# Kernel optimization log

Measured on AMD Instinct MI355X. Metric: run time of the kernel, lower is better.

The kernel has to match this reference:

```python
import jax, jax.numpy as jnp
import numpy as np

# Haar (db1) decomposition filters, pywt convention
_S = 1.0 / np.sqrt(2.0)
# dec_lo = [s, s], dec_hi = [-s, s]. Each scalar input v becomes signal [v, 0]
# (zero-pad to 2**dwt_level = 2). The single valid DWT coeff (mode='zero') is
#   cA = v * dec_lo[1] = v * s ;  cD = v * dec_hi[1] = v * s
CA_COEF = np.float32(_S)   # dec_lo[1]
CD_COEF = np.float32(_S)   # dec_hi[1]

B, N, F, OUT = 8, 20000, 256, 256
WAVELET_FULL_LEN = 2  # len(cA) + len(cD) for level-1 db1 on length-2 signal


def setup_inputs() -> dict:
    key = jax.random.key(0)
    kx, kw, kb, kwo, kbo = jax.random.split(key, 5)
    x = jax.random.normal(kx, (B, N, F), dtype=jnp.float32)
    # per-feature nn.Linear(wavelet_full_len, 1) stacked: weight [F, 2], bias [F]
    lim_nl = 1.0 / np.sqrt(WAVELET_FULL_LEN)
    W_nl = jax.random.uniform(kw, (F, WAVELET_FULL_LEN), jnp.float32, -lim_nl, lim_nl)
    b_nl = jax.random.uniform(kb, (F,), jnp.float32, -lim_nl, lim_nl)
    # linear_out: [out_dim, feat_dim] torch layout, bias [out_dim]
    lim_o = 1.0 / np.sqrt(F)
    W_out = jax.random.uniform(kwo, (OUT, F), jnp.float32, -lim_o, lim_o)
    b_out = jax.random.uniform(kbo, (OUT,), jnp.float32, -lim_o, lim_o)
    return {"x": x, "W_nl": W_nl, "b_nl": b_nl, "W_out": W_out, "b_out": b_out}


def reference(x, W_nl, b_nl, W_out, b_out):
    # Batched wavelet features: for each scalar, coeffs are [cA, cD] = [s*v, s*v]
    # feat_wave: [B, N, F, 2]
    feat_wave = jnp.stack([x * CA_COEF, x * CD_COEF], axis=-1)
    # Per-feature Linear(2, 1), batched over the feature dim
    agg_nl = jnp.einsum("bnfk,fk->bnf", feat_wave, W_nl) + b_nl  # [B, N, F]
    # Output linear (dropout is identity in eval)
    out = jnp.einsum("bnf,of->bno", agg_nl, W_out) + b_out  # [B, N, OUT]
    return out
```

## Files before the change

kernel.cpp:

```cpp
#include <hip/hip_runtime.h>

typedef __bf16 bf16x8 __attribute__((ext_vector_type(8)));
typedef __bf16 bf16x4 __attribute__((ext_vector_type(4)));
typedef float f32x4 __attribute__((ext_vector_type(4)));

__device__ __forceinline__ unsigned short f2b(float f) {
    unsigned int u = __float_as_uint(f);
    return (unsigned short)((u + 0x7fffu + ((u >> 16) & 1u)) >> 16);
}

__global__ __launch_bounds__(256) void wk_prep(
    const float* __restrict__ Wnl, const float* __restrict__ bnl,
    const float* __restrict__ Wout, const float* __restrict__ bout,
    unsigned short* __restrict__ wfrag, float* __restrict__ wbias) {
    int b = blockIdx.x, tid = threadIdx.x;
    if (b < 256) {
        int t = b * 256 + tid;
        int j = t & 7;
        int lane = (t >> 3) & 63;
        int ks = (t >> 9) & 7;
        int ct = t >> 12;
        int f = ks * 32 + ((lane >> 4) << 3) + j;
        int o = ct * 16 + (lane & 15);
        float c = 0.70710678f * (Wnl[2 * f] + Wnl[2 * f + 1]);
        wfrag[t] = f2b(c * Wout[o * 256 + f]);
    } else {
        int o = tid;
        const float4* wr = (const float4*)(Wout + o * 256);
        const float4* bn = (const float4*)bnl;
        float s = 0.f;
        #pragma unroll 4
        for (int i = 0; i < 64; ++i) {
            float4 a = bn[i], b4 = wr[i];
            s += a.x * b4.x + a.y * b4.y + a.z * b4.z + a.w * b4.w;
        }
        wbias[o] = bout[o] + s;
    }
}

__global__ __launch_bounds__(512, 4) void wk_main(
    const float* __restrict__ x, const unsigned short* __restrict__ wfrag,
    const float* __restrict__ wbias, float* __restrict__ out) {
    const int tid  = threadIdx.x;
    const int lane = tid & 63;
    const int w    = tid >> 6;
    const int m    = lane & 15;
    const int quad = lane >> 4;

    __shared__ char Xlds[2][18432];

    const int b  = blockIdx.x;
    const int t0 = (b * 5000) >> 9;
    const int t1 = ((b + 1) * 5000) >> 9;

    int4  Wf[2][8];
    f32x4 bias[2];
    {
        const int4* ws = (const int4*)wfrag;
        #pragma unroll
        for (int c2 = 0; c2 < 2; ++c2) {
            #pragma unroll
            for (int ks = 0; ks < 8; ++ks)
                Wf[c2][ks] = ws[(((2 * w + c2) * 8 + ks) << 6) + lane];
            bias[c2] = *(const f32x4*)(wbias + (2 * w + c2) * 16 + quad * 4);
        }
    }

    f32x4 sbuf[4];
    #define LOADT(T)                                                          \
        {                                                                     \
            const f32x4* xt = (const f32x4*)x + (size_t)(T) * 2048;           \
            _Pragma("unroll")                                                 \
            for (int s = 0; s < 4; ++s)                                       \
                sbuf[s] = xt[s * 512 + w * 64 + lane];                        \
        }

    LOADT(t0);
    int p = 0;
    for (int t = t0; t < t1; ++t) {
        {
            char* dst = Xlds[p] + w * 576 + lane * 8;
            #pragma unroll
            for (int s = 0; s < 4; ++s) {
                f32x4 u = sbuf[s];
                bf16x4 h;
                h[0] = (__bf16)u[0]; h[1] = (__bf16)u[1];
                h[2] = (__bf16)u[2]; h[3] = (__bf16)u[3];
                *(bf16x4*)(dst + s * 4608) = h;
            }
        }
        if (t + 1 < t1) LOADT(t + 1);
        asm volatile("s_waitcnt lgkmcnt(0)" ::: "memory");
        __builtin_amdgcn_s_barrier();
        __builtin_amdgcn_sched_barrier(0);

        const char* src = Xlds[p] + m * 576 + quad * 16;
        #pragma unroll
        for (int mt = 0; mt < 2; ++mt) {
            f32x4 a0 = bias[0], a1 = bias[1];
            #pragma unroll
            for (int ks = 0; ks < 8; ++ks) {
                bf16x8 afr = *(const bf16x8*)(src + mt * 9216 + ks * 64);
                a0 = __builtin_amdgcn_mfma_f32_16x16x32_bf16(
                    __builtin_bit_cast(bf16x8, Wf[0][ks]), afr, a0, 0, 0, 0);
                a1 = __builtin_amdgcn_mfma_f32_16x16x32_bf16(
                    __builtin_bit_cast(bf16x8, Wf[1][ks]), afr, a1, 0, 0, 0);
            }
            float* op = out + (size_t)(t * 32 + mt * 16 + m) * 256 + w * 32 + quad * 4;
            *(f32x4*)op        = a0;
            *(f32x4*)(op + 16) = a1;
        }
        p ^= 1;
    }
    #undef LOADT
}

extern "C" void kernel_launch(void* const* d_in, const int* in_sizes, int n_in,
                              void* d_out, int out_size, void* d_ws, size_t ws_size,
                              hipStream_t stream) {
    const float* x    = (const float*)d_in[0];
    const float* Wnl  = (const float*)d_in[1];
    const float* bnl  = (const float*)d_in[2];
    const float* Wout = (const float*)d_in[3];
    const float* bout = (const float*)d_in[4];

    unsigned short* wfrag = (unsigned short*)d_ws;
    float* wbias = (float*)((char*)d_ws + 131072);

    wk_prep<<<257, 256, 0, stream>>>(Wnl, bnl, Wout, bout, wfrag, wbias);
    wk_main<<<512, 512, 0, stream>>>(x, wfrag, wbias, (float*)d_out);
}
```

Measured before the change: 302.4 us.

## Prefetch two tiles ahead and stage outputs through LDS for coalesced stores

Doubles the register prefetch depth so global loads of x are issued two tiles ahead, using two alternating register buffers and a manually unrolled loop. MFMA results are written to a swizzled LDS buffer and then read back, so each wave stores full contiguous rows of the output instead of scattered 16-byte fragments. This aims to hide load latency and coalesce the dominant output writes, at the cost of an extra barrier per tile, 32KB more LDS per block (which may lower occupancy), and more registers. The prefetch of t0+1 is unconditional, which could read past the block's range when it has only one tile.

```diff
diff --git a/kernel.cpp b/kernel.cpp
--- a/kernel.cpp
+++ b/kernel.cpp
@@ -48,6 +48,7 @@
     const int quad = lane >> 4;
 
     __shared__ char Xlds[2][18432];
+    __shared__ char Olds[32768];
 
     const int b  = blockIdx.x;
     const int t0 = (b * 5000) >> 9;
@@ -66,52 +67,87 @@
         }
     }
 
-    f32x4 sbuf[4];
-    #define LOADT(T)                                                          \
+    f32x4 sbufA[4], sbufB[4];
+    #define LOADT(SB, T)                                                      \
         {                                                                     \
             const f32x4* xt = (const f32x4*)x + (size_t)(T) * 2048;           \
             _Pragma("unroll")                                                 \
             for (int s = 0; s < 4; ++s)                                       \
-                sbuf[s] = xt[s * 512 + w * 64 + lane];                        \
+                SB[s] = xt[s * 512 + w * 64 + lane];                          \
         }
 
-    LOADT(t0);
+    LOADT(sbufA, t0);
+    LOADT(sbufB, t0 + 1);
+
     int p = 0;
-    for (int t = t0; t < t1; ++t) {
-        {
-            char* dst = Xlds[p] + w * 576 + lane * 8;
-            #pragma unroll
-            for (int s = 0; s < 4; ++s) {
-                f32x4 u = sbuf[s];
-                bf16x4 h;
-                h[0] = (__bf16)u[0]; h[1] = (__bf16)u[1];
-                h[2] = (__bf16)u[2]; h[3] = (__bf16)u[3];
-                *(bf16x4*)(dst + s * 4608) = h;
-            }
-        }
-        if (t + 1 < t1) LOADT(t + 1);
-        asm volatile("s_waitcnt lgkmcnt(0)" ::: "memory");
-        __builtin_amdgcn_s_barrier();
-        __builtin_amdgcn_sched_barrier(0);
+    int t = t0;
 
-        const char* src = Xlds[p] + m * 576 + quad * 16;
-        #pragma unroll
-        for (int mt = 0; mt < 2; ++mt) {
-            f32x4 a0 = bias[0], a1 = bias[1];
-            #pragma unroll
-            for (int ks = 0; ks < 8; ++ks) {
-                bf16x8 afr = *(const bf16x8*)(src + mt * 9216 + ks * 64);
-                a0 = __builtin_amdgcn_mfma_f32_16x16x32_bf16(
-                    __builtin_bit_cast(bf16x8, Wf[0][ks]), afr, a0, 0, 0, 0);
-                a1 = __builtin_amdgcn_mfma_f32_16x16x32_bf16(
-                    __builtin_bit_cast(bf16x8, Wf[1][ks]), afr, a1, 0, 0, 0);
-            }
-            float* op = out + (size_t)(t * 32 + mt * 16 + m) * 256 + w * 32 + quad * 4;
-            *(f32x4*)op        = a0;
-            *(f32x4*)(op + 16) = a1;
-        }
-        p ^= 1;
+    #define STEP(SB)                                                          \
+    {                                                                         \
+              \
+        {                                                                     \
+            char* dst = Xlds[p] + w * 576 + lane * 8;                         \
+            _Pragma("unroll")                                                 \
+            for (int s = 0; s < 4; ++s) {                                     \
+                f32x4 u = SB[s];                                              \
+                bf16x4 h;                                                     \
+                h[0] = (__bf16)u[0]; h[1] = (__bf16)u[1];                     \
+                h[2] = (__bf16)u[2]; h[3] = (__bf16)u[3];                     \
+                *(bf16x4*)(dst + s * 4608) = h;                               \
+            }                                                                 \
+        }                                                                     \
+        if (t + 2 < t1) LOADT(SB, t + 2);               \
+        asm volatile("s_waitcnt lgkmcnt(0)" ::: "memory");                    \
+        __builtin_amdgcn_s_barrier();                                         \
+        __builtin_amdgcn_sched_barrier(0);                                    \
+                              \
+        {                                                                     \
+            const char* src = Xlds[p] + m * 576 + quad * 16;                  \
+            _Pragma("unroll")                                                 \
+            for (int mt = 0; mt < 2; ++mt) {                                  \
+                f32x4 a0 = bias[0], a1 = bias[1];                             \
+                _Pragma("unroll")                                             \
+                for (int ks = 0; ks < 8; ++ks) {                              \
+                    bf16x8 afr = *(const bf16x8*)(src + mt * 9216 + ks * 64); \
+                    a0 = __builtin_amdgcn_mfma_f32_16x16x32_bf16(             \
+                        __builtin_bit_cast(bf16x8, Wf[0][ks]), afr, a0,0,0,0);\
+                    a1 = __builtin_amdgcn_mfma_f32_16x16x32_bf16(             \
+                        __builtin_bit_cast(bf16x8, Wf[1][ks]), afr, a1,0,0,0);\
+                }                                                             \
+                const int S0 = 2 * w, S1 = 2 * w + 1;                         \
+                *(f32x4*)(Olds + ((S0 * 2048 + mt * 1024 + lane * 16)         \
+                                  ^ ((S0 & 7) << 4))) = a0;                   \
+                *(f32x4*)(Olds + ((S1 * 2048 + mt * 1024 + lane * 16)         \
+                                  ^ ((S1 & 7) << 4))) = a1;                   \
+            }                                                                 \
+        }                                                                     \
+        asm volatile("s_waitcnt lgkmcnt(0)" ::: "memory");                    \
+        __builtin_amdgcn_s_barrier();                                         \
+        __builtin_amdgcn_sched_barrier(0);                                    \
+          \
+        {                                                                     \
+            float* ob = out + (size_t)t * 8192;                               \
+            _Pragma("unroll")                                                 \
+            for (int it = 0; it < 4; ++it) {                                  \
+                const int R = it * 8 + w;                \
+                const int mtr = R >> 4, mr = R & 15;                          \
+                const int Sr = lane >> 2;                                     \
+                f32x4 v = *(const f32x4*)(Olds +                              \
+                    ((Sr * 2048 + mtr * 1024 + ((lane & 3) * 16 + mr) * 16)   \
+                     ^ ((Sr & 7) << 4)));                                     \
+                *(f32x4*)(ob + it * 2048 + tid * 4) = v;                      \
+            }                                                                 \
+        }                                                                     \
+        p ^= 1;                                                               \
     }
+
+    for (;;) {
+        STEP(sbufA);
+        if (++t == t1) break;
+        STEP(sbufB);
+        if (++t == t1) break;
+    }
+    #undef STEP
     #undef LOADT
 }
 
```

Result: slower. 309.4 us (+2.3%).
